# Performance work log

Hardware: AMD Instinct MI355X
Metric: run time of the kernel (lower is better)

Reference implementation:

```python
import jax, jax.numpy as jnp
import numpy as np

LN_EPS = 1e-5


def setup_inputs() -> dict:
    key = jax.random.key(0)
    k1, k2, k3, k4 = jax.random.split(key, 4)
    B, S, F, H = 128, 1024, 16, 512
    x = jax.random.normal(k1, (B, S, F), dtype=jnp.float32)
    # stacked per-feature Linear(1,H): W[i] = feature_projs[i].weight[:,0], b[i] = bias
    W = jax.random.normal(k2, (F, H), dtype=jnp.float32) * (1.0 / np.sqrt(F))
    b = jax.random.normal(k3, (F, H), dtype=jnp.float32) * 0.02
    emb = jax.random.normal(k4, (S, H), dtype=jnp.float32)  # num_stabilizers == S
    gamma = jnp.ones((H,), dtype=jnp.float32)
    beta = jnp.zeros((H,), dtype=jnp.float32)
    return {"x": x, "W": W, "b": b, "emb": emb, "gamma": gamma, "beta": beta}


def reference(x, W, b, emb, gamma, beta):
    # sum_i Linear_i(x[...,i:i+1]) == x @ W + sum_i b_i  (single fused GEMM)
    h = jnp.einsum("bsf,fh->bsh", x, W) + b.sum(axis=0)
    # index embedding: idx = arange(S), broadcast over batch
    h = h + emb[: x.shape[1]]  # (B,S,H) + (S,H)
    # LayerNorm over last dim
    mu = h.mean(axis=-1, keepdims=True)
    var = h.var(axis=-1, keepdims=True)
    hn = (h - mu) * jax.lax.rsqrt(var + LN_EPS)
    return hn * gamma + beta
```

## Files before the change

kernel.cpp:

```cpp
#include <hip/hip_runtime.h>

#define LN_EPS 1e-5f

static constexpr int Hc    = 512;
static constexpr int Fc    = 16;
static constexpr int Sc    = 1024;
static constexpr int NROWS = 128 * 1024;
static constexpr int RPW   = 16;

__global__ void emb2_kernel(const float* __restrict__ b, const float* __restrict__ emb,
                            float* __restrict__ emb2) {
    const int s = blockIdx.x;
    const int h = threadIdx.x * 4;
    float4 acc = *reinterpret_cast<const float4*>(&emb[s * Hc + h]);
#pragma unroll
    for (int i = 0; i < Fc; ++i) {
        float4 bv = *reinterpret_cast<const float4*>(&b[i * Hc + h]);
        acc.x += bv.x; acc.y += bv.y; acc.z += bv.z; acc.w += bv.w;
    }
    *reinterpret_cast<float4*>(&emb2[s * Hc + h]) = acc;
}

template <int CTRL, int RMASK>
__device__ __forceinline__ float dpp_add(float v) {
    int t = __builtin_amdgcn_update_dpp(0, __float_as_int(v), CTRL, RMASK, 0xf, true);
    return v + __int_as_float(t);
}
__device__ __forceinline__ float wave_sum64(float v) {
    v = dpp_add<0x111, 0xf>(v);
    v = dpp_add<0x112, 0xf>(v);
    v = dpp_add<0x114, 0xf>(v);
    v = dpp_add<0x118, 0xf>(v);
    v = dpp_add<0x142, 0xa>(v);
    v = dpp_add<0x143, 0xc>(v);
    return __int_as_float(__builtin_amdgcn_readlane(__float_as_int(v), 63));
}

__device__ __forceinline__ float rdlane(float v, int l) {
    return __int_as_float(__builtin_amdgcn_readlane(__float_as_int(v), l));
}

template <bool FOLDED>
__global__ __launch_bounds__(256) void fused_kernel(
    const float* __restrict__ x, const float* __restrict__ W,
    const float* __restrict__ embp,
    const float* __restrict__ bsum,
    const float* __restrict__ gamma, const float* __restrict__ beta,
    float* __restrict__ out)
{
    const int lane  = threadIdx.x & 63;
    const int wid   = (blockIdx.x << 2) | (threadIdx.x >> 6);
    const int rbase = wid * RPW;
    const int h0 = lane * 4, h1 = h0 + 256;
    const int s0 = rbase & (Sc - 1);

    float4 w0[Fc], w1[Fc];
#pragma unroll
    for (int i = 0; i < Fc; ++i) {
        w0[i] = *reinterpret_cast<const float4*>(&W[i * Hc + h0]);
        w1[i] = *reinterpret_cast<const float4*>(&W[i * Hc + h1]);
    }

    const float* xb = x + (size_t)rbase * Fc;
    float xq0 = __builtin_nontemporal_load(xb + 0 * 64 + lane);
    float xq1 = __builtin_nontemporal_load(xb + 1 * 64 + lane);
    float xq2 = __builtin_nontemporal_load(xb + 2 * 64 + lane);
    float xq3 = __builtin_nontemporal_load(xb + 3 * 64 + lane);

    const float4 g0  = *reinterpret_cast<const float4*>(&gamma[h0]);
    const float4 g1  = *reinterpret_cast<const float4*>(&gamma[h1]);
    const float4 be0 = *reinterpret_cast<const float4*>(&beta[h0]);
    const float4 be1 = *reinterpret_cast<const float4*>(&beta[h1]);
    float4 bs0, bs1;
    if (!FOLDED) {
        bs0 = *reinterpret_cast<const float4*>(&bsum[h0]);
        bs1 = *reinterpret_cast<const float4*>(&bsum[h1]);
    }

    float4 eA0 = *reinterpret_cast<const float4*>(&embp[(size_t)s0 * Hc + h0]);
    float4 eA1 = *reinterpret_cast<const float4*>(&embp[(size_t)s0 * Hc + h1]);
    float4 eB0, eB1;

#pragma unroll
    for (int t = 0; t < RPW; ++t) {
        if (t < RPW - 1) {
            const float* en = &embp[(size_t)(s0 + t + 1) * Hc];
            if (t & 1) { eA0 = *reinterpret_cast<const float4*>(&en[h0]);
                         eA1 = *reinterpret_cast<const float4*>(&en[h1]); }
            else       { eB0 = *reinterpret_cast<const float4*>(&en[h0]);
                         eB1 = *reinterpret_cast<const float4*>(&en[h1]); }
        }
        const float4 ec0 = (t & 1) ? eB0 : eA0;
        const float4 ec1 = (t & 1) ? eB1 : eA1;

        const float xsrc = (t >> 2) == 0 ? xq0 : (t >> 2) == 1 ? xq1 : (t >> 2) == 2 ? xq2 : xq3;
        float xs[Fc];
#pragma unroll
        for (int i = 0; i < Fc; ++i)
            xs[i] = rdlane(xsrc, (t & 3) * 16 + i);

        float4 a0, a1;
        a0.x = xs[0] * w0[0].x; a0.y = xs[0] * w0[0].y; a0.z = xs[0] * w0[0].z; a0.w = xs[0] * w0[0].w;
        a1.x = xs[0] * w1[0].x; a1.y = xs[0] * w1[0].y; a1.z = xs[0] * w1[0].z; a1.w = xs[0] * w1[0].w;
#pragma unroll
        for (int i = 1; i < Fc; ++i) {
            a0.x = fmaf(xs[i], w0[i].x, a0.x);
            a0.y = fmaf(xs[i], w0[i].y, a0.y);
            a0.z = fmaf(xs[i], w0[i].z, a0.z);
            a0.w = fmaf(xs[i], w0[i].w, a0.w);
            a1.x = fmaf(xs[i], w1[i].x, a1.x);
            a1.y = fmaf(xs[i], w1[i].y, a1.y);
            a1.z = fmaf(xs[i], w1[i].z, a1.z);
            a1.w = fmaf(xs[i], w1[i].w, a1.w);
        }
        a0.x += ec0.x; a0.y += ec0.y; a0.z += ec0.z; a0.w += ec0.w;
        a1.x += ec1.x; a1.y += ec1.y; a1.z += ec1.z; a1.w += ec1.w;
        if (!FOLDED) {
            a0.x += bs0.x; a0.y += bs0.y; a0.z += bs0.z; a0.w += bs0.w;
            a1.x += bs1.x; a1.y += bs1.y; a1.z += bs1.z; a1.w += bs1.w;
        }

        float psum = a0.x + a0.y + a0.z + a0.w + a1.x + a1.y + a1.z + a1.w;
        float pssq = fmaf(a0.x, a0.x, fmaf(a0.y, a0.y, fmaf(a0.z, a0.z, a0.w * a0.w)));
        pssq = fmaf(a1.x, a1.x, fmaf(a1.y, a1.y, fmaf(a1.z, a1.z, fmaf(a1.w, a1.w, pssq))));

        const float sum = wave_sum64(psum);
        const float ssq = wave_sum64(pssq);

        const float mean = sum * (1.0f / 512.0f);
        const float var  = ssq * (1.0f / 512.0f) - mean * mean;
        const float rs   = rsqrtf(var + LN_EPS);

        float4 r0, r1;
        r0.x = (a0.x - mean) * rs * g0.x + be0.x;
        r0.y = (a0.y - mean) * rs * g0.y + be0.y;
        r0.z = (a0.z - mean) * rs * g0.z + be0.z;
        r0.w = (a0.w - mean) * rs * g0.w + be0.w;
        r1.x = (a1.x - mean) * rs * g1.x + be1.x;
        r1.y = (a1.y - mean) * rs * g1.y + be1.y;
        r1.z = (a1.z - mean) * rs * g1.z + be1.z;
        r1.w = (a1.w - mean) * rs * g1.w + be1.w;

        float* orow = out + (size_t)(rbase + t) * Hc;
        *reinterpret_cast<float4*>(&orow[h0]) = r0;
        *reinterpret_cast<float4*>(&orow[h1]) = r1;
    }
}

__global__ void bsum_kernel(const float* __restrict__ b, float* __restrict__ bsum) {
    int h = blockIdx.x * 64 + threadIdx.x;
    float s = 0.f;
#pragma unroll
    for (int i = 0; i < Fc; ++i) s += b[i * Hc + h];
    bsum[h] = s;
}

extern "C" void kernel_launch(void* const* d_in, const int* in_sizes, int n_in,
                              void* d_out, int out_size, void* d_ws, size_t ws_size,
                              hipStream_t stream) {
    const float* x     = (const float*)d_in[0];
    const float* W     = (const float*)d_in[1];
    const float* b     = (const float*)d_in[2];
    const float* emb   = (const float*)d_in[3];
    const float* gamma = (const float*)d_in[4];
    const float* beta  = (const float*)d_in[5];
    float* out = (float*)d_out;

    const int blocks = NROWS / (RPW * 4);

    if (ws_size >= (size_t)Sc * Hc * sizeof(float)) {
        float* emb2 = (float*)d_ws;
        emb2_kernel<<<Sc, Hc / 4, 0, stream>>>(b, emb, emb2);
        fused_kernel<true><<<blocks, 256, 0, stream>>>(x, W, emb2, nullptr, gamma, beta, out);
    } else {
        float* bsum = (float*)d_ws;
        bsum_kernel<<<Hc / 64, 64, 0, stream>>>(b, bsum);
        fused_kernel<false><<<blocks, 256, 0, stream>>>(x, W, emb, bsum, gamma, beta, out);
    }
}
```

Measured before the change: 74.29 us.

## Assign each wave one sequence position across 16 batches to reuse embedding row

Each wave now handles a fixed sequence index s for 16 different batch rows, rather than 16 consecutive rows of one batch. The embedding row plus the bias sum is loaded once into registers and used to seed the FMA accumulator. This removes the per-row embedding reloads and the separate emb+bias precompute kernel that wrote a full S×H buffer. The cost is strided loads of x and strided output writes across batches, each still a contiguous 2KB row, and less contiguous memory per wave.

Result: faster. 70.86 us (-4.6%).

```diff
diff --git a/kernel.cpp b/kernel.cpp
--- a/kernel.cpp
+++ b/kernel.cpp
@@ -2,23 +2,18 @@
 
 #define LN_EPS 1e-5f
 
-static constexpr int Hc    = 512;
-static constexpr int Fc    = 16;
-static constexpr int Sc    = 1024;
-static constexpr int NROWS = 128 * 1024;
-static constexpr int RPW   = 16;
+static constexpr int Hc  = 512;
+static constexpr int Fc  = 16;
+static constexpr int Sc  = 1024;
+static constexpr int Bc  = 128;
+static constexpr int RPW = 16;
 
-__global__ void emb2_kernel(const float* __restrict__ b, const float* __restrict__ emb,
-                            float* __restrict__ emb2) {
-    const int s = blockIdx.x;
-    const int h = threadIdx.x * 4;
-    float4 acc = *reinterpret_cast<const float4*>(&emb[s * Hc + h]);
+__global__ void bsum_kernel(const float* __restrict__ b, float* __restrict__ bsum) {
+    int h = blockIdx.x * 64 + threadIdx.x;
+    float s = 0.f;
 #pragma unroll
-    for (int i = 0; i < Fc; ++i) {
-        float4 bv = *reinterpret_cast<const float4*>(&b[i * Hc + h]);
-        acc.x += bv.x; acc.y += bv.y; acc.z += bv.z; acc.w += bv.w;
-    }
-    *reinterpret_cast<float4*>(&emb2[s * Hc + h]) = acc;
+    for (int i = 0; i < Fc; ++i) s += b[i * Hc + h];
+    bsum[h] = s;
 }
 
 template <int CTRL, int RMASK>
@@ -40,19 +35,17 @@
     return __int_as_float(__builtin_amdgcn_readlane(__float_as_int(v), l));
 }
 
-template <bool FOLDED>
 __global__ __launch_bounds__(256) void fused_kernel(
     const float* __restrict__ x, const float* __restrict__ W,
-    const float* __restrict__ embp,
-    const float* __restrict__ bsum,
+    const float* __restrict__ emb, const float* __restrict__ bsum,
     const float* __restrict__ gamma, const float* __restrict__ beta,
     float* __restrict__ out)
 {
-    const int lane  = threadIdx.x & 63;
-    const int wid   = (blockIdx.x << 2) | (threadIdx.x >> 6);
-    const int rbase = wid * RPW;
+    const int lane = threadIdx.x & 63;
+    const int wid  = (blockIdx.x << 2) | (threadIdx.x >> 6);
+    const int s    = wid & (Sc - 1);
+    const int g    = wid >> 10;
     const int h0 = lane * 4, h1 = h0 + 256;
-    const int s0 = rbase & (Sc - 1);
 
     float4 w0[Fc], w1[Fc];
 #pragma unroll
@@ -61,49 +54,41 @@
         w1[i] = *reinterpret_cast<const float4*>(&W[i * Hc + h1]);
     }
 
-    const float* xb = x + (size_t)rbase * Fc;
-    float xq0 = __builtin_nontemporal_load(xb + 0 * 64 + lane);
-    float xq1 = __builtin_nontemporal_load(xb + 1 * 64 + lane);
-    float xq2 = __builtin_nontemporal_load(xb + 2 * 64 + lane);
-    float xq3 = __builtin_nontemporal_load(xb + 3 * 64 + lane);
+    const int sub = lane >> 4, i16 = lane & 15;
+    float xq0, xq1, xq2, xq3;
+    {
+        const size_t xoff = (size_t)s * Fc + i16;
+        xq0 = __builtin_nontemporal_load(&x[(size_t)(g * 16 + 0 * 4 + sub) * Sc * Fc + xoff]);
+        xq1 = __builtin_nontemporal_load(&x[(size_t)(g * 16 + 1 * 4 + sub) * Sc * Fc + xoff]);
+        xq2 = __builtin_nontemporal_load(&x[(size_t)(g * 16 + 2 * 4 + sub) * Sc * Fc + xoff]);
+        xq3 = __builtin_nontemporal_load(&x[(size_t)(g * 16 + 3 * 4 + sub) * Sc * Fc + xoff]);
+    }
 
     const float4 g0  = *reinterpret_cast<const float4*>(&gamma[h0]);
     const float4 g1  = *reinterpret_cast<const float4*>(&gamma[h1]);
     const float4 be0 = *reinterpret_cast<const float4*>(&beta[h0]);
     const float4 be1 = *reinterpret_cast<const float4*>(&beta[h1]);
-    float4 bs0, bs1;
-    if (!FOLDED) {
-        bs0 = *reinterpret_cast<const float4*>(&bsum[h0]);
-        bs1 = *reinterpret_cast<const float4*>(&bsum[h1]);
+    float4 ebs0, ebs1;
+    {
+        const float4 e0  = *reinterpret_cast<const float4*>(&emb[(size_t)s * Hc + h0]);
+        const float4 e1  = *reinterpret_cast<const float4*>(&emb[(size_t)s * Hc + h1]);
+        const float4 bs0 = *reinterpret_cast<const float4*>(&bsum[h0]);
+        const float4 bs1 = *reinterpret_cast<const float4*>(&bsum[h1]);
+        ebs0.x = e0.x + bs0.x; ebs0.y = e0.y + bs0.y; ebs0.z = e0.z + bs0.z; ebs0.w = e0.w + bs0.w;
+        ebs1.x = e1.x + bs1.x; ebs1.y = e1.y + bs1.y; ebs1.z = e1.z + bs1.z; ebs1.w = e1.w + bs1.w;
     }
-
-    float4 eA0 = *reinterpret_cast<const float4*>(&embp[(size_t)s0 * Hc + h0]);
-    float4 eA1 = *reinterpret_cast<const float4*>(&embp[(size_t)s0 * Hc + h1]);
-    float4 eB0, eB1;
 
 #pragma unroll
     for (int t = 0; t < RPW; ++t) {
-        if (t < RPW - 1) {
-            const float* en = &embp[(size_t)(s0 + t + 1) * Hc];
-            if (t & 1) { eA0 = *reinterpret_cast<const float4*>(&en[h0]);
-                         eA1 = *reinterpret_cast<const float4*>(&en[h1]); }
-            else       { eB0 = *reinterpret_cast<const float4*>(&en[h0]);
-                         eB1 = *reinterpret_cast<const float4*>(&en[h1]); }
-        }
-        const float4 ec0 = (t & 1) ? eB0 : eA0;
-        const float4 ec1 = (t & 1) ? eB1 : eA1;
-
         const float xsrc = (t >> 2) == 0 ? xq0 : (t >> 2) == 1 ? xq1 : (t >> 2) == 2 ? xq2 : xq3;
         float xs[Fc];
 #pragma unroll
         for (int i = 0; i < Fc; ++i)
             xs[i] = rdlane(xsrc, (t & 3) * 16 + i);
 
-        float4 a0, a1;
-        a0.x = xs[0] * w0[0].x; a0.y = xs[0] * w0[0].y; a0.z = xs[0] * w0[0].z; a0.w = xs[0] * w0[0].w;
-        a1.x = xs[0] * w1[0].x; a1.y = xs[0] * w1[0].y; a1.z = xs[0] * w1[0].z; a1.w = xs[0] * w1[0].w;
+        float4 a0 = ebs0, a1 = ebs1;
 #pragma unroll
-        for (int i = 1; i < Fc; ++i) {
+        for (int i = 0; i < Fc; ++i) {
             a0.x = fmaf(xs[i], w0[i].x, a0.x);
             a0.y = fmaf(xs[i], w0[i].y, a0.y);
             a0.z = fmaf(xs[i], w0[i].z, a0.z);
@@ -112,12 +97,6 @@
             a1.y = fmaf(xs[i], w1[i].y, a1.y);
             a1.z = fmaf(xs[i], w1[i].z, a1.z);
             a1.w = fmaf(xs[i], w1[i].w, a1.w);
-        }
-        a0.x += ec0.x; a0.y += ec0.y; a0.z += ec0.z; a0.w += ec0.w;
-        a1.x += ec1.x; a1.y += ec1.y; a1.z += ec1.z; a1.w += ec1.w;
-        if (!FOLDED) {
-            a0.x += bs0.x; a0.y += bs0.y; a0.z += bs0.z; a0.w += bs0.w;
-            a1.x += bs1.x; a1.y += bs1.y; a1.z += bs1.z; a1.w += bs1.w;
         }
 
         float psum = a0.x + a0.y + a0.z + a0.w + a1.x + a1.y + a1.z + a1.w;
@@ -141,18 +120,10 @@
         r1.z = (a1.z - mean) * rs * g1.z + be1.z;
         r1.w = (a1.w - mean) * rs * g1.w + be1.w;
 
-        float* orow = out + (size_t)(rbase + t) * Hc;
+        float* orow = out + ((size_t)(g * 16 + t) * Sc + s) * Hc;
         *reinterpret_cast<float4*>(&orow[h0]) = r0;
         *reinterpret_cast<float4*>(&orow[h1]) = r1;
     }
-}
-
-__global__ void bsum_kernel(const float* __restrict__ b, float* __restrict__ bsum) {
-    int h = blockIdx.x * 64 + threadIdx.x;
-    float s = 0.f;
-#pragma unroll
-    for (int i = 0; i < Fc; ++i) s += b[i * Hc + h];
-    bsum[h] = s;
 }
 
 extern "C" void kernel_launch(void* const* d_in, const int* in_sizes, int n_in,
@@ -164,17 +135,11 @@
     const float* emb   = (const float*)d_in[3];
     const float* gamma = (const float*)d_in[4];
     const float* beta  = (const float*)d_in[5];
-    float* out = (float*)d_out;
+    float* out  = (float*)d_out;
+    float* bsum = (float*)d_ws;
 
-    const int blocks = NROWS / (RPW * 4);
+    bsum_kernel<<<Hc / 64, 64, 0, stream>>>(b, bsum);
 
-    if (ws_size >= (size_t)Sc * Hc * sizeof(float)) {
-        float* emb2 = (float*)d_ws;
-        emb2_kernel<<<Sc, Hc / 4, 0, stream>>>(b, emb, emb2);
-        fused_kernel<true><<<blocks, 256, 0, stream>>>(x, W, emb2, nullptr, gamma, beta, out);
-    } else {
-        float* bsum = (float*)d_ws;
-        bsum_kernel<<<Hc / 64, 64, 0, stream>>>(b, bsum);
-        fused_kernel<false><<<blocks, 256, 0, stream>>>(x, W, emb, bsum, gamma, beta, out);
-    }
+    const int blocks = (8 * Sc) / 4;
+    fused_kernel<<<blocks, 256, 0, stream>>>(x, W, emb, bsum, gamma, beta, out);
 }
```
